# Performance work log

Measured on AMD Instinct MI355X. Metric: run time of the kernel, lower is better.

Reference implementation:

```python
import jax, jax.numpy as jnp
import numpy as np
from jax import lax

# ---- helpers ----

def conv2d(x, w, b, p):
    # x: NCHW, w: OIHW
    y = lax.conv_general_dilated(x, w, (1, 1), [(p, p), (p, p)],
                                 dimension_numbers=('NCHW', 'OIHW', 'NCHW'))
    return y + b.reshape(1, -1, 1, 1)


def bn_eval(x, g, be, m, v):
    # BatchNorm2d in inference mode, eps=1e-5 (torch default)
    inv = lax.rsqrt(v + 1e-5)
    return (x - m.reshape(1, -1, 1, 1)) * (g * inv).reshape(1, -1, 1, 1) + be.reshape(1, -1, 1, 1)


def gelu(x):
    return jax.nn.gelu(x, approximate=False)  # torch nn.GELU default is exact


def up2(x):
    # bilinear upsample x2 with align_corners=True (nn.UpsamplingBilinear2d)
    B, C, H, W = x.shape
    def coords(n):
        N = 2 * n
        s = jnp.arange(N, dtype=jnp.float32) * (float(n - 1) / float(N - 1))
        i0 = jnp.floor(s).astype(jnp.int32)
        i1 = jnp.minimum(i0 + 1, n - 1)
        wgt = (s - i0.astype(jnp.float32)).astype(x.dtype)
        return i0, i1, wgt
    y0, y1, wy = coords(H)
    x0, x1, wx = coords(W)
    r = x[:, :, y0, :] * (1.0 - wy)[:, None] + x[:, :, y1, :] * wy[:, None]
    r = r[:, :, :, x0] * (1.0 - wx) + r[:, :, :, x1] * wx
    return r


def avg_pool2(x):
    return lax.reduce_window(x, 0.0, lax.add, (1, 1, 2, 2), (1, 1, 2, 2), 'VALID') * 0.25


def max_pool2(x):
    return lax.reduce_window(x, -jnp.inf, lax.max, (1, 1, 2, 2), (1, 1, 2, 2), 'VALID')


def dilate3(x):
    # cv2.dilate with ones(3,3), 1 iteration == 3x3 max filter, stride 1, SAME
    return lax.reduce_window(x, -jnp.inf, lax.max, (1, 1, 3, 3), (1, 1, 1, 1), 'SAME')


def ap_mp(x1, x2):
    # AP_MP: L2 norm over channels of (avgpool(x1) - maxpool(x2)) -> [B,1,h,w]
    d = avg_pool2(x1) - max_pool2(x2)
    return jnp.sqrt(jnp.sum(d * d, axis=1, keepdims=True))


def setup_inputs() -> dict:
    key = jax.random.key(0)
    ks = jax.random.split(key, 40)
    B, C1, C2, H, W = 8, 64, 128, 192, 192
    h, w = H // 2, W // 2
    f = jnp.float32

    def conv_w(k, o, i, kh):
        return jax.random.normal(k, (o, i, kh, kh), f) * (1.0 / np.sqrt(i * kh * kh))

    def bn_p(k, c):
        k1, k2, k3, k4 = jax.random.split(k, 4)
        return (jax.random.uniform(k1, (c,), f, 0.5, 1.5),
                jax.random.normal(k2, (c,), f) * 0.1,
                jax.random.normal(k3, (c,), f) * 0.1,
                jax.random.uniform(k4, (c,), f, 0.5, 1.5))

    g_up, be_up, m_up, v_up = bn_p(ks[10], C1)
    g_d1, be_d1, m_d1, v_d1 = bn_p(ks[11], C1)
    g_d2, be_d2, m_d2, v_d2 = bn_p(ks[12], C1)
    g_d3, be_d3, m_d3, v_d3 = bn_p(ks[13], C1)

    return {
        'x': jax.random.normal(ks[0], (B, C1, H, W), f),
        'small_x': jax.random.normal(ks[1], (B, C2, h, w), f),
        'in_map': jax.random.normal(ks[2], (B, 1, h, w), f),
        'W_up': conv_w(ks[3], C1, C2, 7), 'b_up': jax.random.normal(ks[4], (C1,), f) * 0.01,
        'g_up': g_up, 'be_up': be_up, 'm_up': m_up, 'v_up': v_up,
        'W_c2': conv_w(ks[5], C1, C1, 3), 'b_c2': jax.random.normal(ks[6], (C1,), f) * 0.01,
        'W_d1': conv_w(ks[7], C1, 2 * C1, 3), 'b_d1': jax.random.normal(ks[8], (C1,), f) * 0.01,
        'g_d1': g_d1, 'be_d1': be_d1, 'm_d1': m_d1, 'v_d1': v_d1,
        'W_d2': conv_w(ks[14], C1, C1, 3), 'b_d2': jax.random.normal(ks[15], (C1,), f) * 0.01,
        'g_d2': g_d2, 'be_d2': be_d2, 'm_d2': m_d2, 'v_d2': v_d2,
        'W_d3': conv_w(ks[16], C1, C1, 3), 'b_d3': jax.random.normal(ks[17], (C1,), f) * 0.01,
        'g_d3': g_d3, 'be_d3': be_d3, 'm_d3': m_d3, 'v_d3': v_d3,
        'W_out': conv_w(ks[18], 1, C1, 7), 'b_out': jax.random.normal(ks[19], (1,), f) * 0.01,
        'beta': jnp.ones((1,), f),
    }


def reference(x, small_x, in_map,
              W_up, b_up, g_up, be_up, m_up, v_up,
              W_c2, b_c2,
              W_d1, b_d1, g_d1, be_d1, m_d1, v_d1,
              W_d2, b_d2, g_d2, be_d2, m_d2, v_d2,
              W_d3, b_d3, g_d3, be_d3, m_d3, v_d3,
              W_out, b_out, beta):
    # self.up: conv7x7 C2->C1, BN, GELU, bilinear up x2
    small = up2(gelu(bn_eval(conv2d(small_x, W_up, b_up, 3), g_up, be_up, m_up, v_up)))

    # AP_MP based uncertainty map (conv_context_* outputs are unused in forward)
    diff_map = ap_mp(small, x) + ap_mp(x, small)         # [B,1,H/2,W/2]

    input_map = jax.nn.sigmoid(up2(in_map))              # [B,1,H,W]
    diff_map = jax.nn.sigmoid(up2(diff_map))             # [B,1,H,W]

    # focus_background=True path: morphological dilation (3x3, 1 iter) minus map
    increase_map = dilate3(input_map) - input_map
    difference_map = dilate3(diff_map) - diff_map
    b_feature = x * (increase_map + difference_map + 1.0)

    fn = conv2d(b_feature, W_c2, b_c2, 1)
    r = jnp.concatenate([small, beta.reshape(()) * fn], axis=1)
    r = gelu(bn_eval(conv2d(r, W_d1, b_d1, 1), g_d1, be_d1, m_d1, v_d1))
    r = gelu(bn_eval(conv2d(r, W_d2, b_d2, 1), g_d2, be_d2, m_d2, v_d2))
    r = gelu(bn_eval(conv2d(r, W_d3, b_d3, 1), g_d3, be_d3, m_d3, v_d3))
    output_map = conv2d(r, W_out, b_out, 3)
    return (r, output_map)
```

## Files before the change

kernel.cpp:

```cpp
#include <hip/hip_runtime.h>
#include <math.h>


#define DI __device__ __forceinline__

typedef __attribute__((ext_vector_type(8))) short short8;
typedef __attribute__((ext_vector_type(4))) float floatx4;

DI float gelu_f(float x) {
  float u = x * (1.5957691216f + 0.0713548162f * x * x);
  return x / (1.0f + __expf(-u));
}

DI unsigned short f2b(float f) {
  unsigned u = __float_as_uint(f);
  u += 0x7FFFu + ((u >> 16) & 1u);
  return (unsigned short)(u >> 16);
}
DI unsigned pack2(float a, float b) {
  return (unsigned)f2b(a) | ((unsigned)f2b(b) << 16);
}
DI float b2f(short s) { return __uint_as_float(((unsigned)(unsigned short)s) << 16); }

__global__ void epi_prep_k(const float* __restrict__ bias,
                           const float* __restrict__ g, const float* __restrict__ be,
                           const float* __restrict__ m, const float* __restrict__ v,
                           const float* __restrict__ betap, int useBN,
                           float* __restrict__ A, float* __restrict__ B) {
  int oc = threadIdx.x;
  if (oc >= 64) return;
  if (useBN) {
    float giv = g[oc] * rsqrtf(v[oc] + 1e-5f);
    A[oc] = giv;
    B[oc] = (bias[oc] - m[oc]) * giv + be[oc];
  } else {
    float bt = betap[0];
    A[oc] = bt;
    B[oc] = bias[oc] * bt;
  }
}

__global__ void frag3_k(const float* __restrict__ W, short* __restrict__ wf,
                        int CIN, int icg0) {
  int i = blockIdx.x * 256 + threadIdx.x;
  if (i >= 18 * 4 * 64 * 8) return;
  int j = i & 7; int lane = (i >> 3) & 63; int nt = (i >> 9) & 3; int s = i >> 11;
  int q = lane >> 4, r16 = lane & 15;
  int tap = s >> 1, ich = s & 1;
  int ky = tap / 3, kx = tap % 3;
  int ic = icg0 + ich * 32 + q * 8 + j;
  int oc = nt * 16 + r16;
  wf[i] = (short)f2b(W[((oc * CIN + ic) * 3 + ky) * 3 + kx]);
}

__global__ void frag_up_k(const float* __restrict__ W, short* __restrict__ wf) {
  int i = blockIdx.x * 256 + threadIdx.x;
  if (i >= 196 * 4 * 64 * 8) return;
  int j = i & 7; int lane = (i >> 3) & 63; int nt = (i >> 9) & 3; int s = i >> 11;
  int q = lane >> 4, r16 = lane & 15;
  int pass = s / 49, tap = s % 49;
  int ky = tap / 7, kx = tap % 7;
  int ic = pass * 32 + q * 8 + j;
  int oc = nt * 16 + r16;
  wf[i] = (short)f2b(W[((oc * 128 + ic) * 7 + ky) * 7 + kx]);
}

__global__ void frag_out_k(const float* __restrict__ W, short* __restrict__ wf) {
  int i = blockIdx.x * 256 + threadIdx.x;
  if (i >= 98 * 64 * 8) return;
  int j = i & 7; int lane = (i >> 3) & 63; int s = i >> 9;
  int q = lane >> 4;
  int ich = s / 49, tap = s - ich * 49;
  int ch = ich * 32 + q * 8 + j;
  int ky = tap / 7, kx = tap - ky * 7;
  wf[i] = (short)f2b(W[ch * 49 + ky * 7 + kx]);
}

__global__ void to_nhwc_k(const float* __restrict__ in, short* __restrict__ out,
                          int C8, int HW, int total) {
  int i = blockIdx.x * 256 + threadIdx.x;
  if (i >= total) return;
  int cu = i % C8; int p = i / C8;
  int b = p / HW; int pix = p % HW;
  const float* src = in + ((size_t)b * C8 * 8 + cu * 8) * HW + pix;
  int4 o;
  unsigned* op = (unsigned*)&o;
  #pragma unroll
  for (int j = 0; j < 4; ++j)
    op[j] = pack2(src[(2 * j) * (size_t)HW], src[(2 * j + 1) * (size_t)HW]);
  *reinterpret_cast<int4*>(out + (size_t)p * C8 * 8 + cu * 8) = o;
}

template <bool TWO_IN, bool SCALE_IN, bool GELU_OUT, bool OUT_NCHW, bool OUT_BOTH>
__global__ __launch_bounds__(256, 3) void conv3h_k(
    const short* __restrict__ inA, const short* __restrict__ inB,
    const short* __restrict__ wfrag,
    const float* __restrict__ Aepi, const float* __restrict__ Bepi,
    const float* __restrict__ scale,
    short* __restrict__ outH, float* __restrict__ outF)
{
  const int H = 192;
  int bi = blockIdx.x;
  int tx = bi % 12, t2 = bi / 12, ty = t2 % 12, b = t2 / 12;
  int x0 = tx * 16, y0 = ty * 16;
  int tid = threadIdx.x;
  int w = tid >> 6, lane = tid & 63, q = lane >> 4, r16 = lane & 15;

  __shared__ __align__(16) short s_in[324 * 72];
  const short8* wf = (const short8*)wfrag;

  floatx4 acc[4][4];
  #pragma unroll
  for (int a = 0; a < 4; ++a)
    #pragma unroll
    for (int c = 0; c < 4; ++c) acc[a][c] = (floatx4){0.f, 0.f, 0.f, 0.f};

  for (int half = 0; half < (TWO_IN ? 2 : 1); ++half) {
    const short* src = half ? inB : inA;
    if (half) __syncthreads();
    for (int u = tid; u < 2592; u += 256) {
      int px = u >> 3, cu = u & 7;
      int yy = px / 18, xx = px - yy * 18;
      int gy = y0 + yy - 1, gx = x0 + xx - 1;
      int4 v = make_int4(0, 0, 0, 0);
      if (gy >= 0 && gy < H && gx >= 0 && gx < H) {
        v = *reinterpret_cast<const int4*>(src + (((size_t)b * H + gy) * H + gx) * 64 + cu * 8);
        if (SCALE_IN) {
          float sc = scale[((size_t)b * H + gy) * H + gx];
          short* sp = (short*)&v;
          #pragma unroll
          for (int j = 0; j < 8; ++j) sp[j] = (short)f2b(b2f(sp[j]) * sc);
        }
      }
      *reinterpret_cast<int4*>(&s_in[px * 72 + cu * 8]) = v;
    }
    __syncthreads();

    const short8* wfh = wf + half * (18 * 4 * 64);
    short8 wcur[4];
    #pragma unroll
    for (int ot = 0; ot < 4; ++ot) wcur[ot] = wfh[ot * 64 + lane];
    #pragma unroll
    for (int s = 0; s < 18; ++s) {
      short8 wnxt[4];
      if (s < 17) {
        #pragma unroll
        for (int ot = 0; ot < 4; ++ot) wnxt[ot] = wfh[((s + 1) * 4 + ot) * 64 + lane];
      }
      int tap = s >> 1, ich = s & 1;
      int ky = tap / 3, kx = tap - ky * 3;
      #pragma unroll
      for (int yt = 0; yt < 4; ++yt) {
        int iy = w * 4 + yt + ky;
        int ix = r16 + kx;
        short8 pfr = *reinterpret_cast<const short8*>(
            &s_in[(iy * 18 + ix) * 72 + ich * 32 + q * 8]);
        #pragma unroll
        for (int ot = 0; ot < 4; ++ot)
          acc[yt][ot] = __builtin_amdgcn_mfma_f32_16x16x32_bf16(wcur[ot], pfr, acc[yt][ot], 0, 0, 0);
      }
      #pragma unroll
      for (int ot = 0; ot < 4; ++ot) wcur[ot] = wnxt[ot];
    }
  }

  #pragma unroll
  for (int ot = 0; ot < 4; ++ot) {
    float4 A4 = *reinterpret_cast<const float4*>(Aepi + ot * 16 + q * 4);
    float4 B4 = *reinterpret_cast<const float4*>(Bepi + ot * 16 + q * 4);
    #pragma unroll
    for (int yt = 0; yt < 4; ++yt) {
      int gy = y0 + w * 4 + yt;
      float v0 = acc[yt][ot][0] * A4.x + B4.x;
      float v1 = acc[yt][ot][1] * A4.y + B4.y;
      float v2 = acc[yt][ot][2] * A4.z + B4.z;
      float v3 = acc[yt][ot][3] * A4.w + B4.w;
      if (GELU_OUT) { v0 = gelu_f(v0); v1 = gelu_f(v1); v2 = gelu_f(v2); v3 = gelu_f(v3); }
      if (OUT_NCHW) {
        int oc = ot * 16 + q * 4;
        size_t base = (((size_t)b * 64 + oc) * H + gy) * H + x0 + r16;
        outF[base] = v0;
        outF[base + (size_t)H * H] = v1;
        outF[base + 2 * (size_t)H * H] = v2;
        outF[base + 3 * (size_t)H * H] = v3;
      }
      if (!OUT_NCHW || OUT_BOTH) {
        uint2 pk;
        pk.x = pack2(v0, v1);
        pk.y = pack2(v2, v3);
        *reinterpret_cast<uint2*>(
            &outH[(((size_t)b * H + gy) * H + x0 + r16) * 64 + ot * 16 + q * 4]) = pk;
      }
    }
  }
}

__global__ __launch_bounds__(256, 3) void conv_up_h_k(
    const short* __restrict__ in,
    const short* __restrict__ wfrag,
    float* __restrict__ part)
{
  const int H = 96;
  int bi = blockIdx.x;
  int pass = bi & 3; int tile = bi >> 2;
  int tx = tile % 6, t2 = tile / 6, ty = t2 % 6, b = t2 / 6;
  int x0 = tx * 16, y0 = ty * 16;
  int tid = threadIdx.x;
  int w = tid >> 6, lane = tid & 63, q = lane >> 4, r16 = lane & 15;

  __shared__ __align__(16) short s_in[484 * 40];
  const short8* wf = (const short8*)wfrag;

  floatx4 acc[4][4];
  #pragma unroll
  for (int a = 0; a < 4; ++a)
    #pragma unroll
    for (int c = 0; c < 4; ++c) acc[a][c] = (floatx4){0.f, 0.f, 0.f, 0.f};

  for (int u = tid; u < 1936; u += 256) {
    int px = u >> 2, cu = u & 3;
    int yy = px / 22, xx = px - yy * 22;
    int gy = y0 + yy - 3, gx = x0 + xx - 3;
    int4 v = make_int4(0, 0, 0, 0);
    if (gy >= 0 && gy < H && gx >= 0 && gx < H)
      v = *reinterpret_cast<const int4*>(
          in + (((size_t)b * H + gy) * H + gx) * 128 + pass * 32 + cu * 8);
    *reinterpret_cast<int4*>(&s_in[px * 40 + cu * 8]) = v;
  }
  __syncthreads();

  const short8* wfp = wf + pass * (49 * 4 * 64);
  short8 wcur[4];
  #pragma unroll
  for (int ot = 0; ot < 4; ++ot) wcur[ot] = wfp[ot * 64 + lane];
  for (int s = 0; s < 49; ++s) {
    short8 wnxt[4];
    if (s < 48) {
      #pragma unroll
      for (int ot = 0; ot < 4; ++ot) wnxt[ot] = wfp[((s + 1) * 4 + ot) * 64 + lane];
    }
    int ky = s / 7, kx = s - ky * 7;
    #pragma unroll
    for (int yt = 0; yt < 4; ++yt) {
      int iy = w * 4 + yt + ky;
      int ix = r16 + kx;
      short8 pfr = *reinterpret_cast<const short8*>(&s_in[(iy * 22 + ix) * 40 + q * 8]);
      #pragma unroll
      for (int ot = 0; ot < 4; ++ot)
        acc[yt][ot] = __builtin_amdgcn_mfma_f32_16x16x32_bf16(wcur[ot], pfr, acc[yt][ot], 0, 0, 0);
    }
    #pragma unroll
    for (int ot = 0; ot < 4; ++ot) wcur[ot] = wnxt[ot];
  }

  float* dst = part + (size_t)pass * 4718592;
  #pragma unroll
  for (int yt = 0; yt < 4; ++yt) {
    int gy = y0 + w * 4 + yt;
    #pragma unroll
    for (int ot = 0; ot < 4; ++ot) {
      float4 o;
      o.x = acc[yt][ot][0]; o.y = acc[yt][ot][1];
      o.z = acc[yt][ot][2]; o.w = acc[yt][ot][3];
      *reinterpret_cast<float4*>(
          &dst[(((size_t)b * H + gy) * H + x0 + r16) * 64 + ot * 16 + q * 4]) = o;
    }
  }
}

__global__ void reduce_up_k(const float* __restrict__ part,
                            const float* __restrict__ A, const float* __restrict__ B,
                            short* __restrict__ out)
{
  int i8 = blockIdx.x * 256 + threadIdx.x;
  if (i8 >= 589824) return;
  size_t base = (size_t)i8 * 8;
  const size_t N = 4718592;
  float s[8];
  #pragma unroll
  for (int j = 0; j < 8; ++j) s[j] = 0.f;
  #pragma unroll
  for (int p = 0; p < 4; ++p) {
    float4 a = *reinterpret_cast<const float4*>(part + p * N + base);
    float4 bq = *reinterpret_cast<const float4*>(part + p * N + base + 4);
    s[0] += a.x; s[1] += a.y; s[2] += a.z; s[3] += a.w;
    s[4] += bq.x; s[5] += bq.y; s[6] += bq.z; s[7] += bq.w;
  }
  int oc0 = (int)(base & 63);
  int4 o;
  unsigned* op = (unsigned*)&o;
  #pragma unroll
  for (int j = 0; j < 4; ++j) {
    float va = gelu_f(s[2 * j] * A[oc0 + 2 * j] + B[oc0 + 2 * j]);
    float vb = gelu_f(s[2 * j + 1] * A[oc0 + 2 * j + 1] + B[oc0 + 2 * j + 1]);
    op[j] = pack2(va, vb);
  }
  *reinterpret_cast<int4*>(out + base) = o;
}

__global__ void up2h_k(const short* __restrict__ in, short* __restrict__ out) {
  int i = blockIdx.x * 256 + threadIdx.x;
  if (i >= 2359296) return;
  int cu = i & 7; int p = i >> 3;
  int x = p % 192; int t = p / 192; int y = t % 192; int b = t / 192;
  const float c95 = 95.0f / 191.0f;
  float sy = y * c95; int y0i = (int)sy; int y1i = min(y0i + 1, 95); float wy = sy - (float)y0i;
  float sx = x * c95; int x0i = (int)sx; int x1i = min(x0i + 1, 95); float wx = sx - (float)x0i;
  const short* base = in + (size_t)b * 96 * 96 * 64;
  int4 a00 = *reinterpret_cast<const int4*>(base + (y0i * 96 + x0i) * 64 + cu * 8);
  int4 a01 = *reinterpret_cast<const int4*>(base + (y0i * 96 + x1i) * 64 + cu * 8);
  int4 a10 = *reinterpret_cast<const int4*>(base + (y1i * 96 + x0i) * 64 + cu * 8);
  int4 a11 = *reinterpret_cast<const int4*>(base + (y1i * 96 + x1i) * 64 + cu * 8);
  const short* s00 = (const short*)&a00; const short* s01 = (const short*)&a01;
  const short* s10 = (const short*)&a10; const short* s11 = (const short*)&a11;
  float w00 = (1.f - wy) * (1.f - wx), w01 = (1.f - wy) * wx;
  float w10 = wy * (1.f - wx), w11 = wy * wx;
  int4 o;
  unsigned* op = (unsigned*)&o;
  #pragma unroll
  for (int j = 0; j < 4; ++j) {
    float va = b2f(s00[2 * j]) * w00 + b2f(s01[2 * j]) * w01 +
               b2f(s10[2 * j]) * w10 + b2f(s11[2 * j]) * w11;
    float vb = b2f(s00[2 * j + 1]) * w00 + b2f(s01[2 * j + 1]) * w01 +
               b2f(s10[2 * j + 1]) * w10 + b2f(s11[2 * j + 1]) * w11;
    op[j] = pack2(va, vb);
  }
  *reinterpret_cast<int4*>(out + (size_t)p * 64 + cu * 8) = o;
}

__global__ void pools_h_k(const short* __restrict__ small, const short* __restrict__ xh,
                          float* __restrict__ out) {
  int i = blockIdx.x * 256 + threadIdx.x;
  if (i >= 73728) return;
  int x96 = i % 96; int y96 = (i / 96) % 96; int b = i / 9216;
  size_t base = (((size_t)b * 192 + 2 * y96) * 192 + 2 * x96) * 64;
  const int RS = 192 * 64;
  float s1 = 0.f, s2 = 0.f;
  for (int cu = 0; cu < 8; ++cu) {
    int4 sa0 = *reinterpret_cast<const int4*>(small + base + cu * 8);
    int4 sa1 = *reinterpret_cast<const int4*>(small + base + 64 + cu * 8);
    int4 sa2 = *reinterpret_cast<const int4*>(small + base + RS + cu * 8);
    int4 sa3 = *reinterpret_cast<const int4*>(small + base + RS + 64 + cu * 8);
    int4 xa0 = *reinterpret_cast<const int4*>(xh + base + cu * 8);
    int4 xa1 = *reinterpret_cast<const int4*>(xh + base + 64 + cu * 8);
    int4 xa2 = *reinterpret_cast<const int4*>(xh + base + RS + cu * 8);
    int4 xa3 = *reinterpret_cast<const int4*>(xh + base + RS + 64 + cu * 8);
    const short* p0 = (const short*)&sa0; const short* p1 = (const short*)&sa1;
    const short* p2 = (const short*)&sa2; const short* p3 = (const short*)&sa3;
    const short* q0 = (const short*)&xa0; const short* q1 = (const short*)&xa1;
    const short* q2 = (const short*)&xa2; const short* q3 = (const short*)&xa3;
    #pragma unroll
    for (int j = 0; j < 8; ++j) {
      float a0 = b2f(p0[j]), a1 = b2f(p1[j]), a2 = b2f(p2[j]), a3 = b2f(p3[j]);
      float b0 = b2f(q0[j]), b1 = b2f(q1[j]), b2 = b2f(q2[j]), b3 = b2f(q3[j]);
      float avgS = 0.25f * (a0 + a1 + a2 + a3);
      float maxS = fmaxf(fmaxf(a0, a1), fmaxf(a2, a3));
      float avgX = 0.25f * (b0 + b1 + b2 + b3);
      float maxX = fmaxf(fmaxf(b0, b1), fmaxf(b2, b3));
      float d1 = avgS - maxX; s1 = fmaf(d1, d1, s1);
      float d2 = avgX - maxS; s2 = fmaf(d2, d2, s2);
    }
  }
  out[((size_t)b * 96 + y96) * 96 + x96] = sqrtf(s1) + sqrtf(s2);
}

template <bool SIG>
__global__ void up2_k(const float* __restrict__ in, float* __restrict__ out, int total) {
  int i = blockIdx.x * 256 + threadIdx.x;
  if (i >= total) return;
  int x = i % 192; int y = (i / 192) % 192; int bc = i / (192 * 192);
  const float c95 = 95.0f / 191.0f;
  float sy = y * c95; int y0 = (int)sy; int y1 = min(y0 + 1, 95); float wy = sy - (float)y0;
  float sx = x * c95; int x0 = (int)sx; int x1 = min(x0 + 1, 95); float wx = sx - (float)x0;
  const float* p = in + (size_t)bc * 96 * 96;
  float v00 = p[y0 * 96 + x0], v01 = p[y0 * 96 + x1];
  float v10 = p[y1 * 96 + x0], v11 = p[y1 * 96 + x1];
  float v = (1.0f - wx) * ((1.0f - wy) * v00 + wy * v10) +
            wx * ((1.0f - wy) * v01 + wy * v11);
  if (SIG) v = 1.0f / (1.0f + expf(-v));
  out[i] = v;
}

__global__ void scale_k(const float* __restrict__ iM, const float* __restrict__ dM,
                        float* __restrict__ out) {
  int i = blockIdx.x * 256 + threadIdx.x;
  if (i >= 8 * 192 * 192) return;
  int x = i % 192; int y = (i / 192) % 192; int b = i / (192 * 192);
  const float* pi = iM + (size_t)b * 192 * 192;
  const float* pd = dM + (size_t)b * 192 * 192;
  float mi = -1e30f, md = -1e30f;
  for (int dy = -1; dy <= 1; ++dy) {
    int yy = y + dy;
    if (yy < 0 || yy >= 192) continue;
    for (int dx = -1; dx <= 1; ++dx) {
      int xx = x + dx;
      if (xx < 0 || xx >= 192) continue;
      mi = fmaxf(mi, pi[yy * 192 + xx]);
      md = fmaxf(md, pd[yy * 192 + xx]);
    }
  }
  out[i] = (mi - pi[y * 192 + x]) + (md - pd[y * 192 + x]) + 1.0f;
}

__global__ __launch_bounds__(256, 4) void conv_out_mfma_k(
    const short* __restrict__ in,
    const short* __restrict__ wfB,
    const float* __restrict__ bias,
    float* __restrict__ out)
{
  const int H = 192;
  int bi = blockIdx.x;
  int tx = bi % 12, t2 = bi / 12, ty = t2 % 12, b = t2 / 12;
  int x0 = tx * 16, y0 = ty * 16;
  int tid = threadIdx.x;
  int w = tid >> 6, lane = tid & 63, q = lane >> 4, r16 = lane & 15;

  __shared__ __align__(16) short s_in[484 * 36];
  const short8* wf = (const short8*)wfB;

  floatx4 acc[4];
  #pragma unroll
  for (int yt = 0; yt < 4; ++yt) acc[yt] = (floatx4){0.f, 0.f, 0.f, 0.f};

  for (int ich = 0; ich < 2; ++ich) {
    if (ich) __syncthreads();
    for (int u = tid; u < 1936; u += 256) {
      int px = u >> 2, cu = u & 3;
      int yy = px / 22, xx = px - yy * 22;
      int gy = y0 + yy - 3, gx = x0 + xx - 3;
      int4 v = make_int4(0, 0, 0, 0);
      if (gy >= 0 && gy < H && gx >= 0 && gx < H)
        v = *reinterpret_cast<const int4*>(
            in + (((size_t)b * H + gy) * H + gx) * 64 + ich * 32 + cu * 8);
      *reinterpret_cast<int4*>(&s_in[px * 36 + cu * 8]) = v;
    }
    __syncthreads();

    const short8* wfi = wf + ich * (49 * 64);
    short8 wcur = wfi[lane];
    for (int s = 0; s < 49; ++s) {
      short8 wnxt;
      if (s < 48) wnxt = wfi[(s + 1) * 64 + lane];
      int ky = s / 7, kx = s - ky * 7;
      #pragma unroll
      for (int yt = 0; yt < 4; ++yt) {
        int iy = w * 4 + yt + ky;
        int ix = r16 + kx;
        short8 pfr = *reinterpret_cast<const short8*>(
            &s_in[(iy * 22 + ix) * 36 + q * 8]);
        acc[yt] = __builtin_amdgcn_mfma_f32_16x16x32_bf16(pfr, wcur, acc[yt], 0, 0, 0);
      }
      wcur = wnxt;
    }
  }

  float b0 = bias[0];
  if (r16 == 0) {
    #pragma unroll
    for (int yt = 0; yt < 4; ++yt) {
      int gy = y0 + w * 4 + yt;
      float4 o = make_float4(acc[yt][0] + b0, acc[yt][1] + b0,
                             acc[yt][2] + b0, acc[yt][3] + b0);
      *reinterpret_cast<float4*>(&out[((size_t)b * H + gy) * H + x0 + q * 4]) = o;
    }
  }
}

extern "C" void kernel_launch(void* const* d_in, const int* in_sizes, int n_in,
                              void* d_out, int out_size, void* d_ws, size_t ws_size,
                              hipStream_t stream) {
  (void)in_sizes; (void)n_in; (void)out_size; (void)ws_size;
  const float* x       = (const float*)d_in[0];
  const float* small_x = (const float*)d_in[1];
  const float* in_map  = (const float*)d_in[2];
  const float* W_up = (const float*)d_in[3];  const float* b_up = (const float*)d_in[4];
  const float* g_up = (const float*)d_in[5];  const float* be_up = (const float*)d_in[6];
  const float* m_up = (const float*)d_in[7];  const float* v_up = (const float*)d_in[8];
  const float* W_c2 = (const float*)d_in[9];  const float* b_c2 = (const float*)d_in[10];
  const float* W_d1 = (const float*)d_in[11]; const float* b_d1 = (const float*)d_in[12];
  const float* g_d1 = (const float*)d_in[13]; const float* be_d1 = (const float*)d_in[14];
  const float* m_d1 = (const float*)d_in[15]; const float* v_d1 = (const float*)d_in[16];
  const float* W_d2 = (const float*)d_in[17]; const float* b_d2 = (const float*)d_in[18];
  const float* g_d2 = (const float*)d_in[19]; const float* be_d2 = (const float*)d_in[20];
  const float* m_d2 = (const float*)d_in[21]; const float* v_d2 = (const float*)d_in[22];
  const float* W_d3 = (const float*)d_in[23]; const float* b_d3 = (const float*)d_in[24];
  const float* g_d3 = (const float*)d_in[25]; const float* be_d3 = (const float*)d_in[26];
  const float* m_d3 = (const float*)d_in[27]; const float* v_d3 = (const float*)d_in[28];
  const float* W_out = (const float*)d_in[29]; const float* b_out = (const float*)d_in[30];
  const float* beta = (const float*)d_in[31];

  const size_t SZ = 18874368;
  float* ws = (float*)d_ws;
  float* partU = ws;
  short* fnh   = (short*)partU;
  short* rh3   = fnh;
  short* r2h   = fnh + 18874368;
  float* p1 = ws + 18874368;
  short* xh  = (short*)p1;
  float* p2 = p1 + 9437184;
  short* sxh = (short*)p2;
  float* p3 = p2 + 4718592;
  short* t0h = (short*)p3;
  short* wf_out = t0h;
  float* p4 = p3 + 2359296;
  short* smallh = (short*)p4;
  float* p5 = p4 + 9437184;
  short* r1h = (short*)p5;
  float* p6 = p5 + 9437184;
  float* diff96 = p6;
  float* iMap   = diff96 + 73728;
  float* dMap   = iMap + 294912;
  float* scaleM = dMap + 294912;
  float* pA = scaleM + 294912;
  float* A_up = pA;        float* B_up = pA + 64;
  float* A_c2 = pA + 128;  float* B_c2 = pA + 192;
  float* A_d1 = pA + 256;  float* B_d1 = pA + 320;
  float* A_d2 = pA + 384;  float* B_d2 = pA + 448;
  float* A_d3 = pA + 512;  float* B_d3 = pA + 576;
  short* wf_up = (short*)(pA + 640);
  short* wf_c2 = wf_up + 401408;
  short* wf_d1 = wf_c2 + 36864;
  short* wf_d2 = wf_d1 + 73728;
  short* wf_d3 = wf_d2 + 36864;

  float* out0 = (float*)d_out;
  float* out1 = out0 + SZ;

  epi_prep_k<<<1, 64, 0, stream>>>(b_up, g_up, be_up, m_up, v_up, nullptr, 1, A_up, B_up);
  epi_prep_k<<<1, 64, 0, stream>>>(b_c2, nullptr, nullptr, nullptr, nullptr, beta, 0, A_c2, B_c2);
  epi_prep_k<<<1, 64, 0, stream>>>(b_d1, g_d1, be_d1, m_d1, v_d1, nullptr, 1, A_d1, B_d1);
  epi_prep_k<<<1, 64, 0, stream>>>(b_d2, g_d2, be_d2, m_d2, v_d2, nullptr, 1, A_d2, B_d2);
  epi_prep_k<<<1, 64, 0, stream>>>(b_d3, g_d3, be_d3, m_d3, v_d3, nullptr, 1, A_d3, B_d3);
  frag_up_k<<<1568, 256, 0, stream>>>(W_up, wf_up);
  frag3_k<<<144, 256, 0, stream>>>(W_c2, wf_c2, 64, 0);
  frag3_k<<<144, 256, 0, stream>>>(W_d1, wf_d1, 128, 0);
  frag3_k<<<144, 256, 0, stream>>>(W_d1, wf_d1 + 36864, 128, 64);
  frag3_k<<<144, 256, 0, stream>>>(W_d2, wf_d2, 64, 0);
  frag3_k<<<144, 256, 0, stream>>>(W_d3, wf_d3, 64, 0);
  to_nhwc_k<<<9216, 256, 0, stream>>>(x, xh, 8, 36864, 2359296);
  to_nhwc_k<<<4608, 256, 0, stream>>>(small_x, sxh, 16, 9216, 1179648);

  conv_up_h_k<<<1152, 256, 0, stream>>>(sxh, wf_up, partU);
  reduce_up_k<<<2304, 256, 0, stream>>>(partU, A_up, B_up, t0h);
  up2h_k<<<9216, 256, 0, stream>>>(t0h, smallh);
  frag_out_k<<<196, 256, 0, stream>>>(W_out, wf_out);

  pools_h_k<<<288, 256, 0, stream>>>(smallh, xh, diff96);
  up2_k<true><<<1152, 256, 0, stream>>>(in_map, iMap, 8 * 192 * 192);
  up2_k<true><<<1152, 256, 0, stream>>>(diff96, dMap, 8 * 192 * 192);
  scale_k<<<1152, 256, 0, stream>>>(iMap, dMap, scaleM);

  conv3h_k<false, true, false, false, false><<<1152, 256, 0, stream>>>(
      xh, nullptr, wf_c2, A_c2, B_c2, scaleM, fnh, nullptr);
  conv3h_k<true, false, true, false, false><<<1152, 256, 0, stream>>>(
      smallh, fnh, wf_d1, A_d1, B_d1, nullptr, r1h, nullptr);
  conv3h_k<false, false, true, false, false><<<1152, 256, 0, stream>>>(
      r1h, nullptr, wf_d2, A_d2, B_d2, nullptr, r2h, nullptr);
  conv3h_k<false, false, true, true, true><<<1152, 256, 0, stream>>>(
      r2h, nullptr, wf_d3, A_d3, B_d3, nullptr, rh3, out0);

  conv_out_mfma_k<<<1152, 256, 0, stream>>>(rh3, wf_out, b_out, out1);
}
```

Before: 785.4 us.

## Retile 3x3 conv to 32x8 tiles and permute output channels for wide stores

The 3x3 implicit-GEMM conv kernel now uses 32-wide by 8-tall spatial tiles, with each wave covering two rows of two 16-pixel halves, in place of 16x16 tiles. Weight fragments are permuted so each lane owns 16 contiguous output channels, which lets the NHWC bf16 epilogue write two 16-byte stores instead of four 8-byte ones. The wider tile cuts the halo overhead per output row and improves NCHW store coalescing. It also raises launch_bounds occupancy on the separate 7x7 up-conv kernel from 3 to 4 blocks, which may cause register spills there.

```diff
diff --git a/kernel.cpp b/kernel.cpp
--- a/kernel.cpp
+++ b/kernel.cpp
@@ -49,7 +49,7 @@
   int tap = s >> 1, ich = s & 1;
   int ky = tap / 3, kx = tap % 3;
   int ic = icg0 + ich * 32 + q * 8 + j;
-  int oc = nt * 16 + r16;
+  int oc = (r16 >> 2) * 16 + nt * 4 + (r16 & 3);
   wf[i] = (short)f2b(W[((oc * CIN + ic) * 3 + ky) * 3 + kx]);
 }
 
@@ -101,12 +101,12 @@
 {
   const int H = 192;
   int bi = blockIdx.x;
-  int tx = bi % 12, t2 = bi / 12, ty = t2 % 12, b = t2 / 12;
-  int x0 = tx * 16, y0 = ty * 16;
+  int tx = bi % 6, t2 = bi / 6, ty = t2 % 24, b = t2 / 24;
+  int x0 = tx * 32, y0 = ty * 8;
   int tid = threadIdx.x;
   int w = tid >> 6, lane = tid & 63, q = lane >> 4, r16 = lane & 15;
 
-  __shared__ __align__(16) short s_in[324 * 72];
+  __shared__ __align__(16) short s_in[340 * 72];
   const short8* wf = (const short8*)wfrag;
 
   floatx4 acc[4][4];
@@ -118,9 +118,9 @@
   for (int half = 0; half < (TWO_IN ? 2 : 1); ++half) {
     const short* src = half ? inB : inA;
     if (half) __syncthreads();
-    for (int u = tid; u < 2592; u += 256) {
+    for (int u = tid; u < 2720; u += 256) {
       int px = u >> 3, cu = u & 7;
-      int yy = px / 18, xx = px - yy * 18;
+      int yy = px / 34, xx = px - yy * 34;
       int gy = y0 + yy - 1, gx = x0 + xx - 1;
       int4 v = make_int4(0, 0, 0, 0);
       if (gy >= 0 && gy < H && gx >= 0 && gx < H) {
@@ -150,52 +150,79 @@
       int tap = s >> 1, ich = s & 1;
       int ky = tap / 3, kx = tap - ky * 3;
       #pragma unroll
-      for (int yt = 0; yt < 4; ++yt) {
-        int iy = w * 4 + yt + ky;
-        int ix = r16 + kx;
-        short8 pfr = *reinterpret_cast<const short8*>(
-            &s_in[(iy * 18 + ix) * 72 + ich * 32 + q * 8]);
+      for (int yt = 0; yt < 2; ++yt) {
         #pragma unroll
-        for (int ot = 0; ot < 4; ++ot)
-          acc[yt][ot] = __builtin_amdgcn_mfma_f32_16x16x32_bf16(wcur[ot], pfr, acc[yt][ot], 0, 0, 0);
+        for (int xh = 0; xh < 2; ++xh) {
+          int iy = w * 2 + yt + ky;
+          int ix = xh * 16 + r16 + kx;
+          short8 pfr = *reinterpret_cast<const short8*>(
+              &s_in[(iy * 34 + ix) * 72 + ich * 32 + q * 8]);
+          #pragma unroll
+          for (int ot = 0; ot < 4; ++ot)
+            acc[yt * 2 + xh][ot] =
+                __builtin_amdgcn_mfma_f32_16x16x32_bf16(wcur[ot], pfr, acc[yt * 2 + xh][ot], 0, 0, 0);
+        }
       }
       #pragma unroll
       for (int ot = 0; ot < 4; ++ot) wcur[ot] = wnxt[ot];
     }
   }
 
+  float4 Af[4], Bf[4];
   #pragma unroll
   for (int ot = 0; ot < 4; ++ot) {
-    float4 A4 = *reinterpret_cast<const float4*>(Aepi + ot * 16 + q * 4);
-    float4 B4 = *reinterpret_cast<const float4*>(Bepi + ot * 16 + q * 4);
-    #pragma unroll
-    for (int yt = 0; yt < 4; ++yt) {
-      int gy = y0 + w * 4 + yt;
-      float v0 = acc[yt][ot][0] * A4.x + B4.x;
-      float v1 = acc[yt][ot][1] * A4.y + B4.y;
-      float v2 = acc[yt][ot][2] * A4.z + B4.z;
-      float v3 = acc[yt][ot][3] * A4.w + B4.w;
-      if (GELU_OUT) { v0 = gelu_f(v0); v1 = gelu_f(v1); v2 = gelu_f(v2); v3 = gelu_f(v3); }
-      if (OUT_NCHW) {
-        int oc = ot * 16 + q * 4;
+    Af[ot] = *reinterpret_cast<const float4*>(Aepi + q * 16 + ot * 4);
+    Bf[ot] = *reinterpret_cast<const float4*>(Bepi + q * 16 + ot * 4);
+  }
+  #pragma unroll
+  for (int yt = 0; yt < 2; ++yt) {
+    int gy = y0 + w * 2 + yt;
+    float va[2][16];
+    #pragma unroll
+    for (int xh = 0; xh < 2; ++xh) {
+      #pragma unroll
+      for (int ot = 0; ot < 4; ++ot) {
+        const int g = yt * 2 + xh;
+        float v0 = acc[g][ot][0] * Af[ot].x + Bf[ot].x;
+        float v1 = acc[g][ot][1] * Af[ot].y + Bf[ot].y;
+        float v2 = acc[g][ot][2] * Af[ot].z + Bf[ot].z;
+        float v3 = acc[g][ot][3] * Af[ot].w + Bf[ot].w;
+        if (GELU_OUT) { v0 = gelu_f(v0); v1 = gelu_f(v1); v2 = gelu_f(v2); v3 = gelu_f(v3); }
+        va[xh][ot * 4 + 0] = v0;
+        va[xh][ot * 4 + 1] = v1;
+        va[xh][ot * 4 + 2] = v2;
+        va[xh][ot * 4 + 3] = v3;
+      }
+    }
+    if (OUT_NCHW) {
+      #pragma unroll
+      for (int idx = 0; idx < 16; ++idx) {
+        int oc = q * 16 + idx;
         size_t base = (((size_t)b * 64 + oc) * H + gy) * H + x0 + r16;
-        outF[base] = v0;
-        outF[base + (size_t)H * H] = v1;
-        outF[base + 2 * (size_t)H * H] = v2;
-        outF[base + 3 * (size_t)H * H] = v3;
-      }
-      if (!OUT_NCHW || OUT_BOTH) {
-        uint2 pk;
-        pk.x = pack2(v0, v1);
-        pk.y = pack2(v2, v3);
-        *reinterpret_cast<uint2*>(
-            &outH[(((size_t)b * H + gy) * H + x0 + r16) * 64 + ot * 16 + q * 4]) = pk;
-      }
-    }
-  }
-}
-
-__global__ __launch_bounds__(256, 3) void conv_up_h_k(
+        outF[base] = va[0][idx];
+        outF[base + 16] = va[1][idx];
+      }
+    }
+    if (!OUT_NCHW || OUT_BOTH) {
+      #pragma unroll
+      for (int xh = 0; xh < 2; ++xh) {
+        int4 o0, o1;
+        unsigned* p0 = (unsigned*)&o0;
+        unsigned* p1 = (unsigned*)&o1;
+        #pragma unroll
+        for (int j = 0; j < 4; ++j) {
+          p0[j] = pack2(va[xh][2 * j], va[xh][2 * j + 1]);
+          p1[j] = pack2(va[xh][8 + 2 * j], va[xh][8 + 2 * j + 1]);
+        }
+        short* dst = outH + (((size_t)b * H + gy) * H + x0 + xh * 16 + r16) * 64 + q * 16;
+        *reinterpret_cast<int4*>(dst) = o0;
+        *reinterpret_cast<int4*>(dst + 8) = o1;
+      }
+    }
+  }
+}
+
+__global__ __launch_bounds__(256, 4) void conv_up_h_k(
     const short* __restrict__ in,
     const short* __restrict__ wfrag,
     float* __restrict__ part)
```

Result: faster. 697.1 us (-11.2%).
